# Optimization experiments

Hardware: AMD Instinct MI355X
Metric: run time of the kernel (lower is better)

The kernel has to match this reference:

```python
import jax, jax.numpy as jnp
import numpy as np

B, S, F, H, DK = 16, 1024, 512, 8, 64
NEG = 999999.0

def setup_inputs() -> dict:
    key = jax.random.key(0)
    ks = jax.random.split(key, 10)
    s = 1.0 / np.sqrt(F)
    inp = {
        'x': jax.random.normal(ks[0], (B, S, F), dtype=jnp.float32),
        'xlen': jax.random.randint(ks[1], (B,), 1, S + 1, dtype=jnp.int32),
        'WQw': jax.random.uniform(ks[2], (H, DK, F), jnp.float32, -s, s),
        'WQb': jax.random.uniform(ks[3], (H, DK), jnp.float32, -s, s),
        'WKw': jax.random.uniform(ks[4], (H, DK, F), jnp.float32, -s, s),
        'WKb': jax.random.uniform(ks[5], (H, DK), jnp.float32, -s, s),
        'WVw': jax.random.uniform(ks[6], (H, DK, F), jnp.float32, -s, s),
        'WVb': jax.random.uniform(ks[7], (H, DK), jnp.float32, -s, s),
        'WOw': jax.random.uniform(ks[8], (F, H * DK), jnp.float32, -1.0/np.sqrt(H*DK), 1.0/np.sqrt(H*DK)),
        'WOb': jax.random.uniform(ks[9], (F,), jnp.float32, -1.0/np.sqrt(H*DK), 1.0/np.sqrt(H*DK)),
    }
    return inp

def reference(x, xlen, WQw, WQb, WKw, WKb, WVw, WVb, WOw, WOb):
    # batched per-head projections: [B,S,F] x [H,DK,F] -> [B,H,S,DK]
    q = jnp.einsum('bsf,hdf->bhsd', x, WQw) + WQb[None, :, None, :]
    k = jnp.einsum('bsf,hdf->bhsd', x, WKw) + WKb[None, :, None, :]
    v = jnp.einsum('bsf,hdf->bhsd', x, WVw) + WVb[None, :, None, :]
    scores = jnp.einsum('bhsd,bhtd->bhst', q, k) / jnp.sqrt(jnp.float32(DK))
    # additive padding mask; original masks key positions >= xlen[j]-1 (off-by-one preserved)
    key_pos = jnp.arange(S)[None, :]                       # [1,S]
    mask = jnp.where(key_pos >= (xlen - 1)[:, None], -NEG, 0.0).astype(jnp.float32)
    scores = scores + mask[:, None, None, :]               # [B,H,S,S]
    attn = jax.nn.softmax(scores, axis=-1)
    z = jnp.einsum('bhst,bhtd->bhsd', attn, v)             # [B,H,S,DK]
    z = jnp.transpose(z, (0, 2, 1, 3)).reshape(B, S, H * DK)  # concat heads
    return z @ WOw.T + WOb
```

## Files before the change

kernel.cpp:

```cpp
#include <hip/hip_runtime.h>

typedef short bf16x8 __attribute__((ext_vector_type(8)));
typedef float f32x4 __attribute__((ext_vector_type(4)));
typedef unsigned short u16;

#define B_   16
#define S_   1024
#define F_   512
#define H_   8
#define DK_  64


__device__ __forceinline__ u16 f2bf(float f) {
    union { float f; unsigned int u; } v; v.f = f;
    return (u16)((v.u + 0x7FFFu + ((v.u >> 16) & 1u)) >> 16);
}
__device__ __forceinline__ float bf2f(u16 h) {
    union { unsigned int u; float f; } v; v.u = ((unsigned int)h) << 16;
    return v.f;
}
__device__ __forceinline__ bf16x8 cvt8(float4 a, float4 b) {
    union { u16 u[8]; bf16x8 v; } r;
    r.u[0] = f2bf(a.x); r.u[1] = f2bf(a.y); r.u[2] = f2bf(a.z); r.u[3] = f2bf(a.w);
    r.u[4] = f2bf(b.x); r.u[5] = f2bf(b.y); r.u[6] = f2bf(b.z); r.u[7] = f2bf(b.w);
    return r.v;
}

__device__ __forceinline__ void gl_lds16(const u16* g, u16* l) {
    __builtin_amdgcn_global_load_lds(
        (const __attribute__((address_space(1))) unsigned int*)g,
        (__attribute__((address_space(3))) unsigned int*)l,
        16, 0, 0);
}

__global__ __launch_bounds__(256) void cvt_all(
    const float* __restrict__ x,
    const float* __restrict__ wq, const float* __restrict__ wk,
    const float* __restrict__ wv, const float* __restrict__ wo,
    const float* __restrict__ bq, const float* __restrict__ bk,
    const float* __restrict__ bv, const float* __restrict__ bo,
    u16* __restrict__ Xbf, u16* __restrict__ Wbase)
{
    const size_t u = (size_t)blockIdx.x * 256 + threadIdx.x;
    const float* src; u16* dst;
    if (u < 1048576)      { src = x  + u * 8;               dst = Xbf + u * 8; }
    else if (u < 1081344) { src = wq + (u - 1048576) * 8;   dst = Wbase + (u - 1048576) * 8; }
    else if (u < 1114112) { src = wk + (u - 1081344) * 8;   dst = Wbase +  262144 + (u - 1081344) * 8; }
    else if (u < 1146880) { src = wv + (u - 1114112) * 8;   dst = Wbase +  524288 + (u - 1114112) * 8; }
    else if (u < 1179648) { src = wo + (u - 1146880) * 8;   dst = Wbase +  786432 + (u - 1146880) * 8; }
    else if (u < 1179712) { src = bq + (u - 1179648) * 8;   dst = Wbase + 1048576 + (u - 1179648) * 8; }
    else if (u < 1179776) { src = bk + (u - 1179712) * 8;   dst = Wbase + 1049088 + (u - 1179712) * 8; }
    else if (u < 1179840) { src = bv + (u - 1179776) * 8;   dst = Wbase + 1049600 + (u - 1179776) * 8; }
    else                  { src = bo + (u - 1179840) * 8;   dst = Wbase + 1050112 + (u - 1179840) * 8; }
    *(bf16x8*)dst = cvt8(*(const float4*)src, *(const float4*)(src + 4));
}

template <int EPI>
__global__ __launch_bounds__(256) void gemm128(
    const u16* __restrict__ A, const u16* __restrict__ Bm,
    const u16* __restrict__ bias, void* __restrict__ out)
{
    __shared__ __align__(16) u16 AsL[4096];
    __shared__ __align__(16) u16 BsL[4096];

    const int t    = threadIdx.x;
    const int wave = t >> 6, lane = t & 63;
    const int l15  = lane & 15, quad = lane >> 4;
    const int wr   = (wave & 1) * 64, wc = (wave >> 1) * 64;
    const int m0   = blockIdx.x * 128, n0 = blockIdx.y * 128;
    const int sr   = t >> 2, scol = (t & 3) * 8;

    f32x4 acc[4][4];
#pragma unroll
    for (int i = 0; i < 4; i++)
#pragma unroll
        for (int j = 0; j < 4; j++) acc[i][j] = {0.f, 0.f, 0.f, 0.f};

    const u16* Ab = A  + (size_t)(m0 + sr) * 512 + scol;
    const u16* Bb = Bm + (size_t)(n0 + sr) * 512 + scol;
    u16* la = &AsL[t * 8];
    u16* lb = &BsL[t * 8];

    for (int k0 = 0; k0 < 512; k0 += 32) {
        gl_lds16(Ab + k0,         la);
        gl_lds16(Ab + 32768 + k0, la + 2048);
        gl_lds16(Bb + k0,         lb);
        gl_lds16(Bb + 32768 + k0, lb + 2048);
        __syncthreads();
        bf16x8 af[4], bfv[4];
#pragma unroll
        for (int i = 0; i < 4; i++) af[i]  = *(const bf16x8*)&AsL[(wr + i * 16 + l15) * 32 + quad * 8];
#pragma unroll
        for (int j = 0; j < 4; j++) bfv[j] = *(const bf16x8*)&BsL[(wc + j * 16 + l15) * 32 + quad * 8];
#pragma unroll
        for (int i = 0; i < 4; i++)
#pragma unroll
            for (int j = 0; j < 4; j++)
                acc[i][j] = __builtin_amdgcn_mfma_f32_16x16x32_bf16(af[i], bfv[j], acc[i][j], 0, 0, 0);
        __syncthreads();
    }

#pragma unroll
    for (int j = 0; j < 4; j++) {
        const int n  = n0 + wc + j * 16 + l15;
        const float bv = bf2f(bias[n]);
        const int hh = n >> 6, d = n & 63;
#pragma unroll
        for (int i = 0; i < 4; i++) {
#pragma unroll
            for (int r = 0; r < 4; r++) {
                const int m = m0 + wr + i * 16 + quad * 4 + r;
                const float val = acc[i][j][r] + bv;
                if (EPI == 0) {
                    const int b = m >> 10, s = m & 1023;
                    ((u16*)out)[((size_t)(b * 8 + hh) * 1024 + s) * 64 + d] = f2bf(val);
                } else if (EPI == 1) {
                    const int b = m >> 10, s = m & 1023;
                    ((u16*)out)[((size_t)(b * 8 + hh) * 64 + d) * 1024 + s] = f2bf(val);
                } else {
                    ((float*)out)[(size_t)m * 512 + n] = val;
                }
            }
        }
    }
}

__global__ __launch_bounds__(256) void attn(
    const u16* __restrict__ Xbf, const u16* __restrict__ Wqbf,
    const u16* __restrict__ bqbf,
    const u16* __restrict__ Kg, const u16* __restrict__ Vt,
    const int* __restrict__ xlen, u16* __restrict__ Z)
{
    __shared__ __align__(16) u16 smem[13824];

    const int t    = threadIdx.x;
    const int wave = t >> 6, lane = t & 63;
    const int l15  = lane & 15, quad = lane >> 4;
    const int bh   = blockIdx.y, b = bh >> 3, h = bh & 7;
    const int bx   = blockIdx.x;
    const int xm1  = xlen[b] - 1;
    const int wm   = (wave & 1) * 32, wn = (wave >> 1) * 32;

    u16* Ks = smem;
    u16* Vs = smem + 4608;
    u16* PQ = smem + 9216 + wave * 1152;

    f32x4 qa[2][2];
#pragma unroll
    for (int i = 0; i < 2; i++)
#pragma unroll
        for (int j = 0; j < 2; j++) qa[i][j] = {0.f, 0.f, 0.f, 0.f};

    const int sr = t >> 2, scol = (t & 3) * 8;
    const u16* Xb = Xbf  + (size_t)(b * 1024 + bx * 64 + sr) * 512 + scol;
    const u16* Wb = Wqbf + (size_t)(h * 64 + sr) * 512 + scol;
    u16* la = &smem[t * 8];
    u16* lb = &smem[2048 + t * 8];

    for (int k0 = 0; k0 < 512; k0 += 32) {
        gl_lds16(Xb + k0, la);
        gl_lds16(Wb + k0, lb);
        __syncthreads();
        bf16x8 af[2], bfv[2];
#pragma unroll
        for (int i = 0; i < 2; i++) af[i]  = *(const bf16x8*)&smem[(wm + i * 16 + l15) * 32 + quad * 8];
#pragma unroll
        for (int j = 0; j < 2; j++) bfv[j] = *(const bf16x8*)&smem[2048 + (wn + j * 16 + l15) * 32 + quad * 8];
#pragma unroll
        for (int i = 0; i < 2; i++)
#pragma unroll
            for (int j = 0; j < 2; j++)
                qa[i][j] = __builtin_amdgcn_mfma_f32_16x16x32_bf16(af[i], bfv[j], qa[i][j], 0, 0, 0);
        __syncthreads();
    }
#pragma unroll
    for (int j = 0; j < 2; j++) {
        const int d  = wn + j * 16 + l15;
        const float bv = bf2f(bqbf[h * 64 + d]);
#pragma unroll
        for (int i = 0; i < 2; i++) {
#pragma unroll
            for (int r = 0; r < 4; r++) {
                const int row = wm + i * 16 + quad * 4 + r;
                smem[9216 + (row >> 4) * 1152 + (row & 15) * 72 + d] = f2bf((qa[i][j][r] + bv) * 0.125f);
            }
        }
    }
    __syncthreads();

    bf16x8 aq[2];
#pragma unroll
    for (int kk = 0; kk < 2; kk++)
        aq[kk] = *(const bf16x8*)&PQ[l15 * 72 + kk * 32 + quad * 8];

    const size_t baseKV = (size_t)bh * (S_ * DK_);
    const bool domask = (xm1 >= 1);
    const int  Slim   = domask ? xm1 : S_;

    f32x4 o[4];
#pragma unroll
    for (int j = 0; j < 4; j++) o[j] = {0.f, 0.f, 0.f, 0.f};
    float li[4] = {0.f, 0.f, 0.f, 0.f};

    const int srow = t >> 3, scl = (t & 7) * 8;

    for (int t0 = 0; t0 < Slim; t0 += 64) {
        *(uint4*)&Ks[srow * 72 + scl]        = *(const uint4*)&Kg[baseKV + (size_t)(t0 + srow) * 64 + scl];
        *(uint4*)&Ks[(srow + 32) * 72 + scl] = *(const uint4*)&Kg[baseKV + (size_t)(t0 + srow + 32) * 64 + scl];
        *(uint4*)&Vs[srow * 72 + scl]        = *(const uint4*)&Vt[baseKV + (size_t)srow * 1024 + t0 + scl];
        *(uint4*)&Vs[(srow + 32) * 72 + scl] = *(const uint4*)&Vt[baseKV + (size_t)(srow + 32) * 1024 + t0 + scl];
        __syncthreads();

        f32x4 sc[4];
#pragma unroll
        for (int nh = 0; nh < 4; nh++) {
            f32x4 s = {0.f, 0.f, 0.f, 0.f};
#pragma unroll
            for (int kk = 0; kk < 2; kk++) {
                bf16x8 bk = *(const bf16x8*)&Ks[(nh * 16 + l15) * 72 + kk * 32 + quad * 8];
                s = __builtin_amdgcn_mfma_f32_16x16x32_bf16(aq[kk], bk, s, 0, 0, 0);
            }
            sc[nh] = s;
        }
        if (domask && (t0 + 64 > xm1)) {
#pragma unroll
            for (int nh = 0; nh < 4; nh++) {
                const float madd = ((t0 + nh * 16 + l15) >= xm1) ? -999999.0f : 0.0f;
#pragma unroll
                for (int r = 0; r < 4; r++) sc[nh][r] += madd;
            }
        }
#pragma unroll
        for (int r = 0; r < 4; r++) {
            float e0 = __expf(sc[0][r]), e1 = __expf(sc[1][r]);
            float e2 = __expf(sc[2][r]), e3 = __expf(sc[3][r]);
            li[r] += (e0 + e1) + (e2 + e3);
            PQ[(quad * 4 + r) * 72 + l15]      = f2bf(e0);
            PQ[(quad * 4 + r) * 72 + 16 + l15] = f2bf(e1);
            PQ[(quad * 4 + r) * 72 + 32 + l15] = f2bf(e2);
            PQ[(quad * 4 + r) * 72 + 48 + l15] = f2bf(e3);
        }
        bf16x8 ap[2];
#pragma unroll
        for (int kk = 0; kk < 2; kk++)
            ap[kk] = *(const bf16x8*)&PQ[l15 * 72 + kk * 32 + quad * 8];
#pragma unroll
        for (int j = 0; j < 4; j++) {
#pragma unroll
            for (int kk = 0; kk < 2; kk++) {
                bf16x8 bv8 = *(const bf16x8*)&Vs[(j * 16 + l15) * 72 + kk * 32 + quad * 8];
                o[j] = __builtin_amdgcn_mfma_f32_16x16x32_bf16(ap[kk], bv8, o[j], 0, 0, 0);
            }
        }
        __syncthreads();
    }

    float linv[4];
#pragma unroll
    for (int r = 0; r < 4; r++) {
        float rs = li[r];
#pragma unroll
        for (int msk = 1; msk < 16; msk <<= 1) rs += __shfl_xor(rs, msk);
        linv[r] = 1.0f / rs;
    }
#pragma unroll
    for (int j = 0; j < 4; j++) {
#pragma unroll
        for (int r = 0; r < 4; r++) {
            const int s = bx * 64 + wave * 16 + quad * 4 + r;
            Z[((size_t)(b * 1024 + s)) * 512 + h * 64 + j * 16 + l15] = f2bf(o[j][r] * linv[r]);
        }
    }
}

extern "C" void kernel_launch(void* const* d_in, const int* in_sizes, int n_in,
                              void* d_out, int out_size, void* d_ws, size_t ws_size,
                              hipStream_t stream)
{
    (void)in_sizes; (void)n_in; (void)out_size; (void)ws_size;

    const float* x    = (const float*)d_in[0];
    const int*   xlen = (const int*)d_in[1];
    const float* WQw  = (const float*)d_in[2];
    const float* WQb  = (const float*)d_in[3];
    const float* WKw  = (const float*)d_in[4];
    const float* WKb  = (const float*)d_in[5];
    const float* WVw  = (const float*)d_in[6];
    const float* WVb  = (const float*)d_in[7];
    const float* WOw  = (const float*)d_in[8];
    const float* WOb  = (const float*)d_in[9];

    const size_t NQ = (size_t)B_ * H_ * S_ * DK_;
    u16* Kb    = (u16*)d_ws;
    u16* Zb    = Kb + NQ;
    u16* Wbase = Zb + NQ;
    u16* WQbf  = Wbase;
    u16* WKbf  = Wbase + 262144;
    u16* WVbf  = Wbase + 524288;
    u16* WObf  = Wbase + 786432;
    u16* bqbf  = Wbase + 1048576;
    u16* bkbf  = Wbase + 1049088;
    u16* bvbf  = Wbase + 1049600;
    u16* bobf  = Wbase + 1050112;
    u16* Xbf = (u16*)d_out;
    u16* Vb  = Xbf + NQ;

    dim3 blk(256);
    cvt_all<<<dim3(4609), blk, 0, stream>>>(x, WQw, WKw, WVw, WOw,
                                            WQb, WKb, WVb, WOb, Xbf, Wbase);

    dim3 gGemm(128, 4);
    gemm128<0><<<gGemm, blk, 0, stream>>>(Xbf, WKbf, bkbf, Kb);
    gemm128<1><<<gGemm, blk, 0, stream>>>(Xbf, WVbf, bvbf, Vb);

    dim3 gAttn(16, 128);
    attn<<<gAttn, blk, 0, stream>>>(Xbf, WQbf, bqbf, Kb, Vb, xlen, Zb);

    gemm128<2><<<gGemm, blk, 0, stream>>>(Zb, WObf, bobf, d_out);
}
```

Baseline: 210.4 us.

## Merge K/V projection GEMMs and enlarge attention query tile to 128 rows

The K and V projection GEMMs are merged into one launch over a contiguous concatenated weight matrix, with the epilogue picking the K or V layout per column. The attention kernel now processes 128 query rows per block (32 per wave) instead of 64, so each K/V tile loaded to shared memory feeds twice as many MFMAs. The grid is flattened with batch as the fastest index, which changes how blocks are scheduled. The cost is more registers and shared memory per block and half as many attention blocks, which may lower occupancy and load balance across varying sequence lengths.

```diff
diff --git a/kernel.cpp b/kernel.cpp
--- a/kernel.cpp
+++ b/kernel.cpp
@@ -55,10 +55,9 @@
     *(bf16x8*)dst = cvt8(*(const float4*)src, *(const float4*)(src + 4));
 }
 
-template <int EPI>
-__global__ __launch_bounds__(256) void gemm128(
+__global__ __launch_bounds__(256) void gemm_kv(
     const u16* __restrict__ A, const u16* __restrict__ Bm,
-    const u16* __restrict__ bias, void* __restrict__ out)
+    const u16* __restrict__ bias, u16* __restrict__ Kout, u16* __restrict__ Vout)
 {
     __shared__ __align__(16) u16 AsL[4096];
     __shared__ __align__(16) u16 BsL[4096];
@@ -104,22 +103,76 @@
     for (int j = 0; j < 4; j++) {
         const int n  = n0 + wc + j * 16 + l15;
         const float bv = bf2f(bias[n]);
-        const int hh = n >> 6, d = n & 63;
+        const int isv = n >> 9;
+        const int nv  = n & 511, hh = nv >> 6, d = nv & 63;
 #pragma unroll
         for (int i = 0; i < 4; i++) {
 #pragma unroll
             for (int r = 0; r < 4; r++) {
                 const int m = m0 + wr + i * 16 + quad * 4 + r;
+                const int b = m >> 10, s = m & 1023;
                 const float val = acc[i][j][r] + bv;
-                if (EPI == 0) {
-                    const int b = m >> 10, s = m & 1023;
-                    ((u16*)out)[((size_t)(b * 8 + hh) * 1024 + s) * 64 + d] = f2bf(val);
-                } else if (EPI == 1) {
-                    const int b = m >> 10, s = m & 1023;
-                    ((u16*)out)[((size_t)(b * 8 + hh) * 64 + d) * 1024 + s] = f2bf(val);
-                } else {
-                    ((float*)out)[(size_t)m * 512 + n] = val;
-                }
+                if (isv) Vout[((size_t)(b * 8 + hh) * 64 + d) * 1024 + s] = f2bf(val);
+                else     Kout[((size_t)(b * 8 + hh) * 1024 + s) * 64 + d] = f2bf(val);
+            }
+        }
+    }
+}
+
+__global__ __launch_bounds__(256) void gemm_out(
+    const u16* __restrict__ A, const u16* __restrict__ Bm,
+    const u16* __restrict__ bias, float* __restrict__ out)
+{
+    __shared__ __align__(16) u16 AsL[4096];
+    __shared__ __align__(16) u16 BsL[4096];
+
+    const int t    = threadIdx.x;
+    const int wave = t >> 6, lane = t & 63;
+    const int l15  = lane & 15, quad = lane >> 4;
+    const int wr   = (wave & 1) * 64, wc = (wave >> 1) * 64;
+    const int m0   = blockIdx.x * 128, n0 = blockIdx.y * 128;
+    const int sr   = t >> 2, scol = (t & 3) * 8;
+
+    f32x4 acc[4][4];
+#pragma unroll
+    for (int i = 0; i < 4; i++)
+#pragma unroll
+        for (int j = 0; j < 4; j++) acc[i][j] = {0.f, 0.f, 0.f, 0.f};
+
+    const u16* Ab = A  + (size_t)(m0 + sr) * 512 + scol;
+    const u16* Bb = Bm + (size_t)(n0 + sr) * 512 + scol;
+    u16* la = &AsL[t * 8];
+    u16* lb = &BsL[t * 8];
+
+    for (int k0 = 0; k0 < 512; k0 += 32) {
+        gl_lds16(Ab + k0,         la);
+        gl_lds16(Ab + 32768 + k0, la + 2048);
+        gl_lds16(Bb + k0,         lb);
+        gl_lds16(Bb + 32768 + k0, lb + 2048);
+        __syncthreads();
+        bf16x8 af[4], bfv[4];
+#pragma unroll
+        for (int i = 0; i < 4; i++) af[i]  = *(const bf16x8*)&AsL[(wr + i * 16 + l15) * 32 + quad * 8];
+#pragma unroll
+        for (int j = 0; j < 4; j++) bfv[j] = *(const bf16x8*)&BsL[(wc + j * 16 + l15) * 32 + quad * 8];
+#pragma unroll
+        for (int i = 0; i < 4; i++)
+#pragma unroll
+            for (int j = 0; j < 4; j++)
+                acc[i][j] = __builtin_amdgcn_mfma_f32_16x16x32_bf16(af[i], bfv[j], acc[i][j], 0, 0, 0);
+        __syncthreads();
+    }
+
+#pragma unroll
+    for (int j = 0; j < 4; j++) {
+        const int n  = n0 + wc + j * 16 + l15;
+        const float bv = bf2f(bias[n]);
+#pragma unroll
+        for (int i = 0; i < 4; i++) {
+#pragma unroll
+            for (int r = 0; r < 4; r++) {
+                const int m = m0 + wr + i * 16 + quad * 4 + r;
+                out[(size_t)m * 512 + n] = acc[i][j][r] + bv;
             }
         }
     }
@@ -131,144 +184,156 @@
     const u16* __restrict__ Kg, const u16* __restrict__ Vt,
     const int* __restrict__ xlen, u16* __restrict__ Z)
 {
-    __shared__ __align__(16) u16 smem[13824];
+    __shared__ __align__(16) u16 smem[18432];
 
     const int t    = threadIdx.x;
     const int wave = t >> 6, lane = t & 63;
     const int l15  = lane & 15, quad = lane >> 4;
-    const int bh   = blockIdx.y, b = bh >> 3, h = bh & 7;
-    const int bx   = blockIdx.x;
+    const int blk  = blockIdx.x;
+    const int b    = blk & 15, h = (blk >> 4) & 7, bx = blk >> 7;
+    const int bh   = b * 8 + h;
+    const int q0   = bx * 128;
     const int xm1  = xlen[b] - 1;
-    const int wm   = (wave & 1) * 32, wn = (wave >> 1) * 32;
-
-    u16* Ks = smem;
-    u16* Vs = smem + 4608;
-    u16* PQ = smem + 9216 + wave * 1152;
-
-    f32x4 qa[2][2];
-#pragma unroll
-    for (int i = 0; i < 2; i++)
-#pragma unroll
-        for (int j = 0; j < 2; j++) qa[i][j] = {0.f, 0.f, 0.f, 0.f};
-
-    const int sr = t >> 2, scol = (t & 3) * 8;
-    const u16* Xb = Xbf  + (size_t)(b * 1024 + bx * 64 + sr) * 512 + scol;
-    const u16* Wb = Wqbf + (size_t)(h * 64 + sr) * 512 + scol;
-    u16* la = &smem[t * 8];
-    u16* lb = &smem[2048 + t * 8];
+    const int PQ   = 9216 + wave * 2304;
+
+    f32x4 qa[2][4];
+#pragma unroll
+    for (int m = 0; m < 2; m++)
+#pragma unroll
+        for (int j = 0; j < 4; j++) qa[m][j] = {0.f, 0.f, 0.f, 0.f};
+
+    const u16* Xg = Xbf  + (size_t)(b * 1024 + q0 + (t >> 2)) * 512 + (t & 3) * 8;
+    const u16* Wg = Wqbf + (size_t)(h * 64 + (t >> 2)) * 512 + (t & 3) * 8;
 
     for (int k0 = 0; k0 < 512; k0 += 32) {
-        gl_lds16(Xb + k0, la);
-        gl_lds16(Wb + k0, lb);
-        __syncthreads();
-        bf16x8 af[2], bfv[2];
-#pragma unroll
-        for (int i = 0; i < 2; i++) af[i]  = *(const bf16x8*)&smem[(wm + i * 16 + l15) * 32 + quad * 8];
-#pragma unroll
-        for (int j = 0; j < 2; j++) bfv[j] = *(const bf16x8*)&smem[2048 + (wn + j * 16 + l15) * 32 + quad * 8];
-#pragma unroll
-        for (int i = 0; i < 2; i++)
-#pragma unroll
-            for (int j = 0; j < 2; j++)
-                qa[i][j] = __builtin_amdgcn_mfma_f32_16x16x32_bf16(af[i], bfv[j], qa[i][j], 0, 0, 0);
-        __syncthreads();
-    }
-#pragma unroll
-    for (int j = 0; j < 2; j++) {
-        const int d  = wn + j * 16 + l15;
-        const float bv = bf2f(bqbf[h * 64 + d]);
-#pragma unroll
-        for (int i = 0; i < 2; i++) {
-#pragma unroll
-            for (int r = 0; r < 4; r++) {
-                const int row = wm + i * 16 + quad * 4 + r;
-                smem[9216 + (row >> 4) * 1152 + (row & 15) * 72 + d] = f2bf((qa[i][j][r] + bv) * 0.125f);
-            }
-        }
-    }
-    __syncthreads();
-
-    bf16x8 aq[2];
-#pragma unroll
-    for (int kk = 0; kk < 2; kk++)
-        aq[kk] = *(const bf16x8*)&PQ[l15 * 72 + kk * 32 + quad * 8];
+        gl_lds16(Xg + k0,             &smem[t * 8]);
+        gl_lds16(Xg + 64 * 512 + k0,  &smem[2048 + t * 8]);
+        gl_lds16(Wg + k0,             &smem[4096 + t * 8]);
+        __syncthreads();
+        bf16x8 af[2], bfv[4];
+#pragma unroll
+        for (int m = 0; m < 2; m++)
+            af[m] = *(const bf16x8*)&smem[(wave * 32 + m * 16 + l15) * 32 + quad * 8];
+#pragma unroll
+        for (int j = 0; j < 4; j++)
+            bfv[j] = *(const bf16x8*)&smem[4096 + (j * 16 + l15) * 32 + quad * 8];
+#pragma unroll
+        for (int m = 0; m < 2; m++)
+#pragma unroll
+            for (int j = 0; j < 4; j++)
+                qa[m][j] = __builtin_amdgcn_mfma_f32_16x16x32_bf16(af[m], bfv[j], qa[m][j], 0, 0, 0);
+        __syncthreads();
+    }
+#pragma unroll
+    for (int j = 0; j < 4; j++) {
+        const float bv = bf2f(bqbf[h * 64 + j * 16 + l15]);
+#pragma unroll
+        for (int m = 0; m < 2; m++)
+#pragma unroll
+            for (int r = 0; r < 4; r++)
+                smem[PQ + (m * 16 + quad * 4 + r) * 72 + j * 16 + l15] =
+                    f2bf((qa[m][j][r] + bv) * 0.125f);
+    }
+    bf16x8 aq[2][2];
+#pragma unroll
+    for (int m = 0; m < 2; m++)
+#pragma unroll
+        for (int kk = 0; kk < 2; kk++)
+            aq[m][kk] = *(const bf16x8*)&smem[PQ + (m * 16 + l15) * 72 + kk * 32 + quad * 8];
 
     const size_t baseKV = (size_t)bh * (S_ * DK_);
     const bool domask = (xm1 >= 1);
     const int  Slim   = domask ? xm1 : S_;
 
-    f32x4 o[4];
-#pragma unroll
-    for (int j = 0; j < 4; j++) o[j] = {0.f, 0.f, 0.f, 0.f};
-    float li[4] = {0.f, 0.f, 0.f, 0.f};
+    f32x4 o[2][4];
+#pragma unroll
+    for (int m = 0; m < 2; m++)
+#pragma unroll
+        for (int j = 0; j < 4; j++) o[m][j] = {0.f, 0.f, 0.f, 0.f};
+    float li[2][4] = {{0.f,0.f,0.f,0.f},{0.f,0.f,0.f,0.f}};
 
     const int srow = t >> 3, scl = (t & 7) * 8;
 
     for (int t0 = 0; t0 < Slim; t0 += 64) {
-        *(uint4*)&Ks[srow * 72 + scl]        = *(const uint4*)&Kg[baseKV + (size_t)(t0 + srow) * 64 + scl];
-        *(uint4*)&Ks[(srow + 32) * 72 + scl] = *(const uint4*)&Kg[baseKV + (size_t)(t0 + srow + 32) * 64 + scl];
-        *(uint4*)&Vs[srow * 72 + scl]        = *(const uint4*)&Vt[baseKV + (size_t)srow * 1024 + t0 + scl];
-        *(uint4*)&Vs[(srow + 32) * 72 + scl] = *(const uint4*)&Vt[baseKV + (size_t)(srow + 32) * 1024 + t0 + scl];
-        __syncthreads();
-
-        f32x4 sc[4];
+        *(uint4*)&smem[srow * 72 + scl]               = *(const uint4*)&Kg[baseKV + (size_t)(t0 + srow) * 64 + scl];
+        *(uint4*)&smem[(srow + 32) * 72 + scl]        = *(const uint4*)&Kg[baseKV + (size_t)(t0 + srow + 32) * 64 + scl];
+        *(uint4*)&smem[4608 + srow * 72 + scl]        = *(const uint4*)&Vt[baseKV + (size_t)srow * 1024 + t0 + scl];
+        *(uint4*)&smem[4608 + (srow + 32) * 72 + scl] = *(const uint4*)&Vt[baseKV + (size_t)(srow + 32) * 1024 + t0 + scl];
+        __syncthreads();
+
+        f32x4 sc[2][4];
 #pragma unroll
         for (int nh = 0; nh < 4; nh++) {
-            f32x4 s = {0.f, 0.f, 0.f, 0.f};
-#pragma unroll
-            for (int kk = 0; kk < 2; kk++) {
-                bf16x8 bk = *(const bf16x8*)&Ks[(nh * 16 + l15) * 72 + kk * 32 + quad * 8];
-                s = __builtin_amdgcn_mfma_f32_16x16x32_bf16(aq[kk], bk, s, 0, 0, 0);
-            }
-            sc[nh] = s;
+            bf16x8 bk0 = *(const bf16x8*)&smem[(nh * 16 + l15) * 72 + quad * 8];
+            bf16x8 bk1 = *(const bf16x8*)&smem[(nh * 16 + l15) * 72 + 32 + quad * 8];
+#pragma unroll
+            for (int m = 0; m < 2; m++) {
+                f32x4 s = {0.f, 0.f, 0.f, 0.f};
+                s = __builtin_amdgcn_mfma_f32_16x16x32_bf16(aq[m][0], bk0, s, 0, 0, 0);
+                s = __builtin_amdgcn_mfma_f32_16x16x32_bf16(aq[m][1], bk1, s, 0, 0, 0);
+                sc[m][nh] = s;
+            }
         }
         if (domask && (t0 + 64 > xm1)) {
 #pragma unroll
             for (int nh = 0; nh < 4; nh++) {
                 const float madd = ((t0 + nh * 16 + l15) >= xm1) ? -999999.0f : 0.0f;
 #pragma unroll
-                for (int r = 0; r < 4; r++) sc[nh][r] += madd;
-            }
-        }
+                for (int m = 0; m < 2; m++)
+#pragma unroll
+                    for (int r = 0; r < 4; r++) sc[m][nh][r] += madd;
+            }
+        }
+#pragma unroll
+        for (int m = 0; m < 2; m++)
+#pragma unroll
+            for (int r = 0; r < 4; r++) {
+                float e0 = __expf(sc[m][0][r]), e1 = __expf(sc[m][1][r]);
+                float e2 = __expf(sc[m][2][r]), e3 = __expf(sc[m][3][r]);
+                li[m][r] += (e0 + e1) + (e2 + e3);
+                const int pr = PQ + (m * 16 + quad * 4 + r) * 72;
+                smem[pr + l15]      = f2bf(e0);
+                smem[pr + 16 + l15] = f2bf(e1);
+                smem[pr + 32 + l15] = f2bf(e2);
+                smem[pr + 48 + l15] = f2bf(e3);
+            }
+        bf16x8 ap[2][2];
+#pragma unroll
+        for (int m = 0; m < 2; m++)
+#pragma unroll
+            for (int kk = 0; kk < 2; kk++)
+                ap[m][kk] = *(const bf16x8*)&smem[PQ + (m * 16 + l15) * 72 + kk * 32 + quad * 8];
+#pragma unroll
+        for (int j = 0; j < 4; j++) {
+#pragma unroll
+            for (int kk = 0; kk < 2; kk++) {
+                bf16x8 bv8 = *(const bf16x8*)&smem[4608 + (j * 16 + l15) * 72 + kk * 32 + quad * 8];
+#pragma unroll
+                for (int m = 0; m < 2; m++)
+                    o[m][j] = __builtin_amdgcn_mfma_f32_16x16x32_bf16(ap[m][kk], bv8, o[m][j], 0, 0, 0);
+            }
+        }
+        __syncthreads();
+    }
+
+#pragma unroll
+    for (int m = 0; m < 2; m++) {
+        float linv[4];
 #pragma unroll
         for (int r = 0; r < 4; r++) {
-            float e0 = __expf(sc[0][r]), e1 = __expf(sc[1][r]);
-            float e2 = __expf(sc[2][r]), e3 = __expf(sc[3][r]);
-            li[r] += (e0 + e1) + (e2 + e3);
-            PQ[(quad * 4 + r) * 72 + l15]      = f2bf(e0);
-            PQ[(quad * 4 + r) * 72 + 16 + l15] = f2bf(e1);
-            PQ[(quad * 4 + r) * 72 + 32 + l15] = f2bf(e2);
-            PQ[(quad * 4 + r) * 72 + 48 + l15] = f2bf(e3);
-        }
-        bf16x8 ap[2];
-#pragma unroll
-        for (int kk = 0; kk < 2; kk++)
-            ap[kk] = *(const bf16x8*)&PQ[l15 * 72 + kk * 32 + quad * 8];
+            float rs = li[m][r];
+#pragma unroll
+            for (int msk = 1; msk < 16; msk <<= 1) rs += __shfl_xor(rs, msk);
+            linv[r] = 1.0f / rs;
+        }
 #pragma unroll
         for (int j = 0; j < 4; j++) {
 #pragma unroll
-            for (int kk = 0; kk < 2; kk++) {
-                bf16x8 bv8 = *(const bf16x8*)&Vs[(j * 16 + l15) * 72 + kk * 32 + quad * 8];
-                o[j] = __builtin_amdgcn_mfma_f32_16x16x32_bf16(ap[kk], bv8, o[j], 0, 0, 0);
-            }
-        }
-        __syncthreads();
-    }
-
-    float linv[4];
-#pragma unroll
-    for (int r = 0; r < 4; r++) {
-        float rs = li[r];
-#pragma unroll
-        for (int msk = 1; msk < 16; msk <<= 1) rs += __shfl_xor(rs, msk);
-        linv[r] = 1.0f / rs;
-    }
-#pragma unroll
-    for (int j = 0; j < 4; j++) {
-#pragma unroll
-        for (int r = 0; r < 4; r++) {
-            const int s = bx * 64 + wave * 16 + quad * 4 + r;
-            Z[((size_t)(b * 1024 + s)) * 512 + h * 64 + j * 16 + l15] = f2bf(o[j][r] * linv[r]);
+            for (int r = 0; r < 4; r++) {
+                const int s = q0 + wave * 32 + m * 16 + quad * 4 + r;
+                Z[((size_t)(b * 1024 + s)) * 512 + h * 64 + j * 16 + l15] =
+                    f2bf(o[m][j][r] * linv[r]);
+            }
         }
     }
 }
@@ -295,12 +360,10 @@
     u16* Zb    = Kb + NQ;
     u16* Wbase = Zb + NQ;
     u16* WQbf  = Wbase;
-    u16* WKbf  = Wbase + 262144;
-    u16* WVbf  = Wbase + 524288;
+    u16* WKVbf = Wbase + 262144;
     u16* WObf  = Wbase + 786432;
     u16* bqbf  = Wbase + 1048576;
-    u16* bkbf  = Wbase + 1049088;
-    u16* bvbf  = Wbase + 1049600;
+    u16* bkvbf = Wbase + 1049088;
     u16* bobf  = Wbase + 1050112;
     u16* Xbf = (u16*)d_out;
     u16* Vb  = Xbf + NQ;
@@ -309,12 +372,9 @@
     cvt_all<<<dim3(4609), blk, 0, stream>>>(x, WQw, WKw, WVw, WOw,
                                             WQb, WKb, WVb, WOb, Xbf, Wbase);
 
-    dim3 gGemm(128, 4);
-    gemm128<0><<<gGemm, blk, 0, stream>>>(Xbf, WKbf, bkbf, Kb);
-    gemm128<1><<<gGemm, blk, 0, stream>>>(Xbf, WVbf, bvbf, Vb);
-
-    dim3 gAttn(16, 128);
-    attn<<<gAttn, blk, 0, stream>>>(Xbf, WQbf, bqbf, Kb, Vb, xlen, Zb);
-
-    gemm128<2><<<gGemm, blk, 0, stream>>>(Zb, WObf, bobf, d_out);
-}
+    gemm_kv<<<dim3(128, 8), blk, 0, stream>>>(Xbf, WKVbf, bkvbf, Kb, Vb);
+
+    attn<<<dim3(1024), blk, 0, stream>>>(Xbf, WQbf, bqbf, Kb, Vb, xlen, Zb);
+
+    gemm_out<<<dim3(128, 4), blk, 0, stream>>>(Zb, WObf, bobf, (float*)d_out);
+}
```

New measurement: 256.7 us. 22.0% more time.
